# Kernel tuning notes

Measured on AMD Instinct MI355X. Metric: run time of the kernel, lower is better.

Reference implementation:

```python
import jax, jax.numpy as jnp
import numpy as np

D_MODEL = 1024
NUM_HEADS = 16
D_K = D_MODEL // NUM_HEADS


def setup_inputs() -> dict:
    key = jax.random.key(0)
    ks = jax.random.split(key, 7)
    B, S = 2, 2048
    scale = 1.0 / np.sqrt(D_MODEL)
    return {
        "Q": jax.random.normal(ks[0], (B, S, D_MODEL), dtype=jnp.float32),
        "K": jax.random.normal(ks[1], (B, S, D_MODEL), dtype=jnp.float32),
        "V": jax.random.normal(ks[2], (B, S, D_MODEL), dtype=jnp.float32),
        "W_q": jax.random.normal(ks[3], (D_MODEL, D_MODEL), dtype=jnp.float32) * scale,
        "W_k": jax.random.normal(ks[4], (D_MODEL, D_MODEL), dtype=jnp.float32) * scale,
        "W_v": jax.random.normal(ks[5], (D_MODEL, D_MODEL), dtype=jnp.float32) * scale,
        "W_o": jax.random.normal(ks[6], (D_MODEL, D_MODEL), dtype=jnp.float32) * scale,
    }


def _split_heads(x):
    B, S, _ = x.shape
    return x.reshape(B, S, NUM_HEADS, D_K).transpose(0, 2, 1, 3)  # [B,H,S,Dk]


def reference(Q, K, V, W_q, W_k, W_v, W_o):
    # nn.Linear(bias=False): x @ W.T
    q = _split_heads(Q @ W_q.T)
    k = _split_heads(K @ W_k.T)
    v = _split_heads(V @ W_v.T)
    scores = jnp.einsum("bhqd,bhkd->bhqk", q, k) / jnp.sqrt(jnp.float32(D_K))
    probs = jax.nn.softmax(scores, axis=-1)
    out = jnp.einsum("bhqk,bhkd->bhqd", probs, v)  # [B,H,S,Dk]
    B, H, S, Dk = out.shape
    out = out.transpose(0, 2, 1, 3).reshape(B, S, H * Dk)
    return out @ W_o.T
```

## Files before the change

kernel.cpp:

```cpp
#include <hip/hip_runtime.h>
#include <cstdint>

#define D_MODEL 1024
#define NH 16
#define DK 64
#define SEQ 2048
#define BATCH 2
#define M_TOT (BATCH * SEQ)

typedef __bf16 bf16x8          __attribute__((ext_vector_type(8)));
typedef unsigned short u16x8   __attribute__((ext_vector_type(8)));
typedef float  f32x4           __attribute__((ext_vector_type(4)));

union pun8 { u16x8 u; bf16x8 b; };

__device__ __forceinline__ f32x4 mfma16(bf16x8 a, bf16x8 b, f32x4 c) {
    return __builtin_amdgcn_mfma_f32_16x16x32_bf16(a, b, c, 0, 0, 0);
}

__device__ __forceinline__ unsigned short f2bf(float f) {
    union { float f; uint32_t u; } v; v.f = f;
    uint32_t u = v.u;
    return (unsigned short)((u + 0x7FFFu + ((u >> 16) & 1u)) >> 16);
}

__device__ __forceinline__ unsigned short f2bf_trunc(float f) {
    union { float f; uint32_t u; } v; v.f = f;
    return (unsigned short)(v.u >> 16);
}

__device__ __forceinline__ void gl_lds16(const unsigned short* g, unsigned short* l) {
    __builtin_amdgcn_global_load_lds(
        (const __attribute__((address_space(1))) void*)g,
        (__attribute__((address_space(3))) void*)l, 16, 0, 0);
}

#define C_EXP2 0.1803368801111204f

__global__ __launch_bounds__(256) void convert_all_kernel(
    const float* __restrict__ Q,  const float* __restrict__ K,
    const float* __restrict__ V,  const float* __restrict__ Wq,
    const float* __restrict__ Wk, const float* __restrict__ Wv,
    const float* __restrict__ Wo,
    unsigned short* __restrict__ Qb,  unsigned short* __restrict__ Kb,
    unsigned short* __restrict__ Vb,  unsigned short* __restrict__ Wqb,
    unsigned short* __restrict__ Wkb, unsigned short* __restrict__ Wvb,
    unsigned short* __restrict__ Wob)
{
    int bid = blockIdx.x;
    const float* src; unsigned short* dst; int base;
    if (bid < 3 * 2048) {
        int r = bid >> 11;
        src  = (r == 0) ? Q  : (r == 1) ? K  : V;
        dst  = (r == 0) ? Qb : (r == 1) ? Kb : Vb;
        base = (bid & 2047) * 2048;
    } else {
        int u = bid - 3 * 2048;
        int r = u >> 9;
        src  = (r == 0) ? Wq  : (r == 1) ? Wk  : (r == 2) ? Wv  : Wo;
        dst  = (r == 0) ? Wqb : (r == 1) ? Wkb : (r == 2) ? Wvb : Wob;
        base = (u & 511) * 2048;
    }
    int i = base + threadIdx.x * 8;
    float4 a = *(const float4*)(src + i);
    float4 b = *(const float4*)(src + i + 4);
    u16x8 o;
    o[0] = f2bf(a.x); o[1] = f2bf(a.y); o[2] = f2bf(a.z); o[3] = f2bf(a.w);
    o[4] = f2bf(b.x); o[5] = f2bf(b.y); o[6] = f2bf(b.z); o[7] = f2bf(b.w);
    *(u16x8*)(dst + i) = o;
}

__global__ __launch_bounds__(256) void qkv_proj_kernel(
    const unsigned short* __restrict__ Q,
    const unsigned short* __restrict__ K,
    const unsigned short* __restrict__ V,
    const unsigned short* __restrict__ Wq,
    const unsigned short* __restrict__ Wk,
    const unsigned short* __restrict__ Wv,
    unsigned short* __restrict__ qb,
    unsigned short* __restrict__ kb,
    unsigned short* __restrict__ vtb)
{
    const int z = blockIdx.z;
    const unsigned short* A  = (z == 0) ? Q  : (z == 1) ? K  : V;
    const unsigned short* Bt = (z == 0) ? Wq : (z == 1) ? Wk : Wv;

    const int m0 = blockIdx.y * 128;
    const int n0 = blockIdx.x * 128;

    __shared__ __align__(16) unsigned short smem[128 * 136];
    unsigned short* As = smem;
    unsigned short* Bs = smem + 128 * 64;
    unsigned short* Cs = smem;

    const int t    = threadIdx.x;
    const int lane = t & 63;
    const int w    = t >> 6;
    const int l15  = lane & 15;
    const int quad = lane >> 4;
    const int wm   = (w >> 1) * 64;
    const int wn   = (w & 1) * 64;

    f32x4 acc[4][4] = {};

    for (int k0 = 0; k0 < D_MODEL; k0 += 64) {
        __syncthreads();
        #pragma unroll
        for (int i = 0; i < 4; i++) {
            int u   = t + i * 256;
            int row = u >> 3;
            int kc  = (u & 7) * 8;
            gl_lds16(&A [(m0 + row) * D_MODEL + k0 + kc], &As[(i * 256 + w * 64) * 8]);
            gl_lds16(&Bt[(n0 + row) * D_MODEL + k0 + kc], &Bs[(i * 256 + w * 64) * 8]);
        }
        __syncthreads();

        #pragma unroll
        for (int kk = 0; kk < 2; kk++) {
            bf16x8 a[4], b[4];
            #pragma unroll
            for (int mi = 0; mi < 4; mi++)
                a[mi] = *(const bf16x8*)(&As[(wm + mi * 16 + l15) * 64 + kk * 32 + quad * 8]);
            #pragma unroll
            for (int ni = 0; ni < 4; ni++)
                b[ni] = *(const bf16x8*)(&Bs[(wn + ni * 16 + l15) * 64 + kk * 32 + quad * 8]);

            #pragma unroll
            for (int mi = 0; mi < 4; mi++)
                #pragma unroll
                for (int ni = 0; ni < 4; ni++)
                    acc[mi][ni] = mfma16(a[mi], b[ni], acc[mi][ni]);
        }
    }

    const float oscale = (z == 0) ? C_EXP2 : 1.0f;
    __syncthreads();
    #pragma unroll
    for (int mi = 0; mi < 4; mi++) {
        #pragma unroll
        for (int ni = 0; ni < 4; ni++) {
            #pragma unroll
            for (int r = 0; r < 4; r++) {
                int rloc = wm + mi * 16 + quad * 4 + r;
                int cloc = wn + ni * 16 + l15;
                int rr = (z == 2) ? cloc : rloc;
                int cc = (z == 2) ? rloc : cloc;
                Cs[rr * 136 + cc] = f2bf(acc[mi][ni][r] * oscale);
            }
        }
    }
    __syncthreads();
    #pragma unroll
    for (int i = 0; i < 8; i++) {
        int u    = t + i * 256;
        int rrow = u >> 4;
        int cc8  = (u & 15) * 8;
        u16x8 val = *(const u16x8*)(&Cs[rrow * 136 + cc8]);
        unsigned short* dst;
        if (z < 2) {
            int m = m0 + rrow, n = n0 + cc8;
            int bi = m >> 11, s = m & (SEQ - 1);
            int hh = n >> 6,  d = n & (DK - 1);
            dst = ((z == 0) ? qb : kb) + (((size_t)(bi * NH + hh) * SEQ + s) * DK + d);
        } else {
            int dglob = n0 + rrow;
            int bi = m0 >> 11, s = (m0 & (SEQ - 1)) + cc8;
            int hh = dglob >> 6, d = dglob & (DK - 1);
            dst = vtb + (((size_t)(bi * NH + hh) * DK + d) * SEQ + s);
        }
        *(u16x8*)dst = val;
    }
}

__global__ __launch_bounds__(256, 2) void attn_kernel(
    const unsigned short* __restrict__ qb,
    const unsigned short* __restrict__ kb,
    const unsigned short* __restrict__ vtb,
    unsigned short* __restrict__ ctx)
{
    const int h  = blockIdx.x;
    const int qt = blockIdx.y;
    const int b  = blockIdx.z;

    const int t    = threadIdx.x;
    const int lane = t & 63;
    const int w    = t >> 6;
    const int l15  = lane & 15;
    const int quad = lane >> 4;

    const unsigned short* qh = qb  + ((b * NH + h) * SEQ) * DK;
    const unsigned short* kh = kb  + ((b * NH + h) * SEQ) * DK;
    const unsigned short* vh = vtb + ((b * NH + h) * DK) * SEQ;

    __shared__ __align__(16) unsigned short p_lds[4][32][72];
    __shared__ __align__(16) unsigned short Ks[128 * 72];
    __shared__ __align__(16) unsigned short Vs[64 * 136];

    const int qrow0 = qt * 128 + w * 32;
    bf16x8 qa[2][2];
    #pragma unroll
    for (int m = 0; m < 2; m++)
        #pragma unroll
        for (int kk = 0; kk < 2; kk++)
            qa[m][kk] = *(const bf16x8*)(&qh[(qrow0 + m * 16 + l15) * DK + kk * 32 + quad * 8]);

    pun8 ones_p;
    #pragma unroll
    for (int i = 0; i < 8; i++) ones_p.u[i] = 0x3F80;
    const bf16x8 ones = ones_p.b;

    f32x4 o[2][4] = {};
    f32x4 lacc[2] = {};

    bf16x8 pa_p[2][2] = {};
    bf16x8 vf_p[4][2] = {};

    for (int kt = 0; kt < SEQ / 128; kt++) {
        __syncthreads();
        #pragma unroll
        for (int i = 0; i < 4; i++) {
            int u   = t + i * 256;
            int row = u >> 3;
            int c8  = (u & 7) * 8;
            *(u16x8*)(&Ks[row * 72 + c8]) =
                *(const u16x8*)(&kh[(kt * 128 + row) * DK + c8]);
        }
        #pragma unroll
        for (int i = 0; i < 4; i++) {
            int u   = t + i * 256;
            int row = u >> 4;
            int c8  = (u & 15) * 8;
            *(u16x8*)(&Vs[row * 136 + c8]) =
                *(const u16x8*)(&vh[row * SEQ + kt * 128 + c8]);
        }
        __syncthreads();

        #pragma unroll
        for (int hh = 0; hh < 2; hh++) {
            bf16x8 kf[4][2];
            #pragma unroll
            for (int nb = 0; nb < 4; nb++) {
                const int krow = hh * 64 + nb * 16 + l15;
                kf[nb][0] = *(const bf16x8*)(&Ks[krow * 72 + quad * 8]);
                kf[nb][1] = *(const bf16x8*)(&Ks[krow * 72 + 32 + quad * 8]);
            }

            f32x4 sacc[2][4] = {};
            __builtin_amdgcn_s_setprio(1);
            #pragma unroll
            for (int m = 0; m < 2; m++)
                #pragma unroll
                for (int nb = 0; nb < 4; nb++) {
                    sacc[m][nb] = mfma16(qa[m][0], kf[nb][0], sacc[m][nb]);
                    sacc[m][nb] = mfma16(qa[m][1], kf[nb][1], sacc[m][nb]);
                }
            __builtin_amdgcn_s_setprio(0);

            bf16x8 vf_c[4][2];
            #pragma unroll
            for (int db = 0; db < 4; db++) {
                vf_c[db][0] = *(const bf16x8*)(&Vs[(db * 16 + l15) * 136 + hh * 64 + quad * 8]);
                vf_c[db][1] = *(const bf16x8*)(&Vs[(db * 16 + l15) * 136 + hh * 64 + 32 + quad * 8]);
            }

            __builtin_amdgcn_s_setprio(1);
            #pragma unroll
            for (int db = 0; db < 4; db++)
                #pragma unroll
                for (int m = 0; m < 2; m++) {
                    o[m][db] = mfma16(pa_p[m][0], vf_p[db][0], o[m][db]);
                    o[m][db] = mfma16(pa_p[m][1], vf_p[db][1], o[m][db]);
                }
            #pragma unroll
            for (int m = 0; m < 2; m++) {
                lacc[m] = mfma16(pa_p[m][0], ones, lacc[m]);
                lacc[m] = mfma16(pa_p[m][1], ones, lacc[m]);
            }
            __builtin_amdgcn_s_setprio(0);

            #pragma unroll
            for (int m = 0; m < 2; m++)
                #pragma unroll
                for (int nb = 0; nb < 4; nb++)
                    #pragma unroll
                    for (int r = 0; r < 4; r++) {
                        float p = exp2f(sacc[m][nb][r]);
                        p_lds[w][m * 16 + quad * 4 + r][nb * 16 + l15] = f2bf_trunc(p);
                    }

            asm volatile("" ::: "memory");

            #pragma unroll
            for (int m = 0; m < 2; m++)
                #pragma unroll
                for (int kk = 0; kk < 2; kk++)
                    pa_p[m][kk] = *(const bf16x8*)(&p_lds[w][m * 16 + l15][kk * 32 + quad * 8]);

            asm volatile("" ::: "memory");

            #pragma unroll
            for (int db = 0; db < 4; db++) {
                vf_p[db][0] = vf_c[db][0];
                vf_p[db][1] = vf_c[db][1];
            }
        }
    }

    __builtin_amdgcn_s_setprio(1);
    #pragma unroll
    for (int db = 0; db < 4; db++)
        #pragma unroll
        for (int m = 0; m < 2; m++) {
            o[m][db] = mfma16(pa_p[m][0], vf_p[db][0], o[m][db]);
            o[m][db] = mfma16(pa_p[m][1], vf_p[db][1], o[m][db]);
        }
    #pragma unroll
    for (int m = 0; m < 2; m++) {
        lacc[m] = mfma16(pa_p[m][0], ones, lacc[m]);
        lacc[m] = mfma16(pa_p[m][1], ones, lacc[m]);
    }
    __builtin_amdgcn_s_setprio(0);

    #pragma unroll
    for (int m = 0; m < 2; m++) {
        const int srow_base = b * SEQ + qt * 128 + w * 32 + m * 16 + quad * 4;
        #pragma unroll
        for (int db = 0; db < 4; db++)
            #pragma unroll
            for (int r = 0; r < 4; r++) {
                float val = o[m][db][r] / lacc[m][r];
                ctx[(srow_base + r) * D_MODEL + h * DK + db * 16 + l15] = f2bf(val);
            }
    }
}

__global__ __launch_bounds__(256) void out_proj_kernel(
    const unsigned short* __restrict__ A,
    const unsigned short* __restrict__ Bt,
    float* __restrict__ out)
{
    const int m0 = blockIdx.y * 64;
    const int n0 = blockIdx.x * 128;

    __shared__ __align__(16) unsigned short As[64 * 64];
    __shared__ __align__(16) unsigned short Bs[128 * 64];

    const int t    = threadIdx.x;
    const int lane = t & 63;
    const int w    = t >> 6;
    const int l15  = lane & 15;
    const int quad = lane >> 4;
    const int wn   = w * 32;

    f32x4 acc[4][2] = {};

    for (int k0 = 0; k0 < D_MODEL; k0 += 64) {
        __syncthreads();
        #pragma unroll
        for (int i = 0; i < 2; i++) {
            int u   = t + i * 256;
            int row = u >> 3;
            int kc  = (u & 7) * 8;
            gl_lds16(&A[(m0 + row) * D_MODEL + k0 + kc], &As[(i * 256 + w * 64) * 8]);
        }
        #pragma unroll
        for (int i = 0; i < 4; i++) {
            int u   = t + i * 256;
            int row = u >> 3;
            int kc  = (u & 7) * 8;
            gl_lds16(&Bt[(n0 + row) * D_MODEL + k0 + kc], &Bs[(i * 256 + w * 64) * 8]);
        }
        __syncthreads();

        #pragma unroll
        for (int kk = 0; kk < 2; kk++) {
            bf16x8 a[4], bfr[2];
            #pragma unroll
            for (int mi = 0; mi < 4; mi++)
                a[mi] = *(const bf16x8*)(&As[(mi * 16 + l15) * 64 + kk * 32 + quad * 8]);
            #pragma unroll
            for (int ni = 0; ni < 2; ni++)
                bfr[ni] = *(const bf16x8*)(&Bs[(wn + ni * 16 + l15) * 64 + kk * 32 + quad * 8]);

            #pragma unroll
            for (int mi = 0; mi < 4; mi++)
                #pragma unroll
                for (int ni = 0; ni < 2; ni++)
                    acc[mi][ni] = mfma16(a[mi], bfr[ni], acc[mi][ni]);
        }
    }

    #pragma unroll
    for (int mi = 0; mi < 4; mi++) {
        #pragma unroll
        for (int ni = 0; ni < 2; ni++) {
            #pragma unroll
            for (int r = 0; r < 4; r++) {
                int m = m0 + mi * 16 + quad * 4 + r;
                int n = n0 + wn + ni * 16 + l15;
                out[m * D_MODEL + n] = acc[mi][ni][r];
            }
        }
    }
}

extern "C" void kernel_launch(void* const* d_in, const int* in_sizes, int n_in,
                              void* d_out, int out_size, void* d_ws, size_t ws_size,
                              hipStream_t stream) {
    const float* Q  = (const float*)d_in[0];
    const float* K  = (const float*)d_in[1];
    const float* V  = (const float*)d_in[2];
    const float* Wq = (const float*)d_in[3];
    const float* Wk = (const float*)d_in[4];
    const float* Wv = (const float*)d_in[5];
    const float* Wo = (const float*)d_in[6];

    const size_t NQ = (size_t)M_TOT * D_MODEL;
    const size_t NW = (size_t)D_MODEL * D_MODEL;

    unsigned short* Qb  = (unsigned short*)d_ws;
    unsigned short* Kb  = Qb  + NQ;
    unsigned short* Vb  = Kb  + NQ;
    unsigned short* Wqb = Vb  + NQ;
    unsigned short* Wkb = Wqb + NW;
    unsigned short* Wvb = Wkb + NW;
    unsigned short* Wob = Wvb + NW;
    unsigned short* qb  = Wob + NW;
    unsigned short* kbf = qb  + NQ;
    unsigned short* vtb = kbf + NQ;
    unsigned short* ctx = vtb + NQ;
    float* out = (float*)d_out;

    convert_all_kernel<<<3 * 2048 + 4 * 512, 256, 0, stream>>>(
        Q, K, V, Wq, Wk, Wv, Wo, Qb, Kb, Vb, Wqb, Wkb, Wvb, Wob);

    dim3 g1(D_MODEL / 128, M_TOT / 128, 3);
    qkv_proj_kernel<<<g1, 256, 0, stream>>>(Qb, Kb, Vb, Wqb, Wkb, Wvb, qb, kbf, vtb);

    dim3 g2(NH, SEQ / 128, BATCH);
    attn_kernel<<<g2, 256, 0, stream>>>(qb, kbf, vtb, ctx);

    dim3 g3(D_MODEL / 128, M_TOT / 64, 1);
    out_proj_kernel<<<g3, 256, 0, stream>>>(ctx, Wob, out);
}
```

Before: 230.8 us.

## Split attention KV range in two and merge partials in output projection

```diff
diff --git a/kernel.cpp b/kernel.cpp
--- a/kernel.cpp
+++ b/kernel.cpp
@@ -27,6 +27,11 @@
 __device__ __forceinline__ unsigned short f2bf_trunc(float f) {
     union { float f; uint32_t u; } v; v.f = f;
     return (unsigned short)(v.u >> 16);
+}
+
+__device__ __forceinline__ float bf2f(unsigned short s) {
+    union { uint32_t u; float f; } v; v.u = ((uint32_t)s) << 16;
+    return v.f;
 }
 
 __device__ __forceinline__ void gl_lds16(const unsigned short* g, unsigned short* l) {
@@ -176,11 +181,16 @@
     const unsigned short* __restrict__ qb,
     const unsigned short* __restrict__ kb,
     const unsigned short* __restrict__ vtb,
-    unsigned short* __restrict__ ctx)
+    unsigned short* __restrict__ u0,
+    unsigned short* __restrict__ u1,
+    float* __restrict__ l0,
+    float* __restrict__ l1)
 {
     const int h  = blockIdx.x;
     const int qt = blockIdx.y;
-    const int b  = blockIdx.z;
+    const int zb = blockIdx.z;
+    const int b  = zb >> 1;
+    const int g  = zb & 1;
 
     const int t    = threadIdx.x;
     const int lane = t & 63;
@@ -188,13 +198,13 @@
     const int l15  = lane & 15;
     const int quad = lane >> 4;
 
-    const unsigned short* qh = qb  + ((b * NH + h) * SEQ) * DK;
-    const unsigned short* kh = kb  + ((b * NH + h) * SEQ) * DK;
-    const unsigned short* vh = vtb + ((b * NH + h) * DK) * SEQ;
+    const unsigned short* qh = qb  + ((size_t)(b * NH + h) * SEQ) * DK;
+    const unsigned short* kh = kb  + ((size_t)(b * NH + h) * SEQ + g * (SEQ / 2)) * DK;
+    const unsigned short* vh = vtb + ((size_t)(b * NH + h) * DK) * SEQ + g * (SEQ / 2);
 
     __shared__ __align__(16) unsigned short p_lds[4][32][72];
-    __shared__ __align__(16) unsigned short Ks[128 * 72];
-    __shared__ __align__(16) unsigned short Vs[64 * 136];
+    __shared__ __align__(16) unsigned short Ks[64 * 72];
+    __shared__ __align__(16) unsigned short Vs[64 * 72];
 
     const int qrow0 = qt * 128 + w * 32;
     bf16x8 qa[2][2];
@@ -215,94 +225,91 @@
     bf16x8 pa_p[2][2] = {};
     bf16x8 vf_p[4][2] = {};
 
-    for (int kt = 0; kt < SEQ / 128; kt++) {
-        __syncthreads();
-        #pragma unroll
-        for (int i = 0; i < 4; i++) {
+    for (int kt = 0; kt < 16; kt++) {
+        __syncthreads();
+        #pragma unroll
+        for (int i = 0; i < 2; i++) {
             int u   = t + i * 256;
             int row = u >> 3;
             int c8  = (u & 7) * 8;
             *(u16x8*)(&Ks[row * 72 + c8]) =
-                *(const u16x8*)(&kh[(kt * 128 + row) * DK + c8]);
-        }
-        #pragma unroll
-        for (int i = 0; i < 4; i++) {
+                *(const u16x8*)(&kh[(kt * 64 + row) * DK + c8]);
+        }
+        #pragma unroll
+        for (int i = 0; i < 2; i++) {
             int u   = t + i * 256;
-            int row = u >> 4;
-            int c8  = (u & 15) * 8;
-            *(u16x8*)(&Vs[row * 136 + c8]) =
-                *(const u16x8*)(&vh[row * SEQ + kt * 128 + c8]);
-        }
-        __syncthreads();
-
-        #pragma unroll
-        for (int hh = 0; hh < 2; hh++) {
-            bf16x8 kf[4][2];
+            int row = u >> 3;
+            int c8  = (u & 7) * 8;
+            *(u16x8*)(&Vs[row * 72 + c8]) =
+                *(const u16x8*)(&vh[row * SEQ + kt * 64 + c8]);
+        }
+        __syncthreads();
+
+        bf16x8 kf[4][2];
+        #pragma unroll
+        for (int nb = 0; nb < 4; nb++) {
+            const int krow = nb * 16 + l15;
+            kf[nb][0] = *(const bf16x8*)(&Ks[krow * 72 + quad * 8]);
+            kf[nb][1] = *(const bf16x8*)(&Ks[krow * 72 + 32 + quad * 8]);
+        }
+
+        f32x4 sacc[2][4] = {};
+        __builtin_amdgcn_s_setprio(1);
+        #pragma unroll
+        for (int m = 0; m < 2; m++)
             #pragma unroll
             for (int nb = 0; nb < 4; nb++) {
-                const int krow = hh * 64 + nb * 16 + l15;
-                kf[nb][0] = *(const bf16x8*)(&Ks[krow * 72 + quad * 8]);
-                kf[nb][1] = *(const bf16x8*)(&Ks[krow * 72 + 32 + quad * 8]);
+                sacc[m][nb] = mfma16(qa[m][0], kf[nb][0], sacc[m][nb]);
+                sacc[m][nb] = mfma16(qa[m][1], kf[nb][1], sacc[m][nb]);
             }
-
-            f32x4 sacc[2][4] = {};
-            __builtin_amdgcn_s_setprio(1);
-            #pragma unroll
-            for (int m = 0; m < 2; m++)
+        __builtin_amdgcn_s_setprio(0);
+
+        bf16x8 vf_c[4][2];
+        #pragma unroll
+        for (int db = 0; db < 4; db++) {
+            vf_c[db][0] = *(const bf16x8*)(&Vs[(db * 16 + l15) * 72 + quad * 8]);
+            vf_c[db][1] = *(const bf16x8*)(&Vs[(db * 16 + l15) * 72 + 32 + quad * 8]);
+        }
+
+        __builtin_amdgcn_s_setprio(1);
+        #pragma unroll
+        for (int db = 0; db < 4; db++)
+            #pragma unroll
+            for (int m = 0; m < 2; m++) {
+                o[m][db] = mfma16(pa_p[m][0], vf_p[db][0], o[m][db]);
+                o[m][db] = mfma16(pa_p[m][1], vf_p[db][1], o[m][db]);
+            }
+        #pragma unroll
+        for (int m = 0; m < 2; m++) {
+            lacc[m] = mfma16(pa_p[m][0], ones, lacc[m]);
+            lacc[m] = mfma16(pa_p[m][1], ones, lacc[m]);
+        }
+        __builtin_amdgcn_s_setprio(0);
+
+        #pragma unroll
+        for (int m = 0; m < 2; m++)
+            #pragma unroll
+            for (int nb = 0; nb < 4; nb++)
                 #pragma unroll
-                for (int nb = 0; nb < 4; nb++) {
-                    sacc[m][nb] = mfma16(qa[m][0], kf[nb][0], sacc[m][nb]);
-                    sacc[m][nb] = mfma16(qa[m][1], kf[nb][1], sacc[m][nb]);
+                for (int r = 0; r < 4; r++) {
+                    float p = exp2f(sacc[m][nb][r]);
+                    p_lds[w][m * 16 + quad * 4 + r][nb * 16 + l15] = f2bf_trunc(p);
                 }
-            __builtin_amdgcn_s_setprio(0);
-
-            bf16x8 vf_c[4][2];
-            #pragma unroll
-            for (int db = 0; db < 4; db++) {
-                vf_c[db][0] = *(const bf16x8*)(&Vs[(db * 16 + l15) * 136 + hh * 64 + quad * 8]);
-                vf_c[db][1] = *(const bf16x8*)(&Vs[(db * 16 + l15) * 136 + hh * 64 + 32 + quad * 8]);
-            }
-
-            __builtin_amdgcn_s_setprio(1);
-            #pragma unroll
-            for (int db = 0; db < 4; db++)
-                #pragma unroll
-                for (int m = 0; m < 2; m++) {
-                    o[m][db] = mfma16(pa_p[m][0], vf_p[db][0], o[m][db]);
-                    o[m][db] = mfma16(pa_p[m][1], vf_p[db][1], o[m][db]);
-                }
-            #pragma unroll
-            for (int m = 0; m < 2; m++) {
-                lacc[m] = mfma16(pa_p[m][0], ones, lacc[m]);
-                lacc[m] = mfma16(pa_p[m][1], ones, lacc[m]);
-            }
-            __builtin_amdgcn_s_setprio(0);
-
-            #pragma unroll
-            for (int m = 0; m < 2; m++)
-                #pragma unroll
-                for (int nb = 0; nb < 4; nb++)
-                    #pragma unroll
-                    for (int r = 0; r < 4; r++) {
-                        float p = exp2f(sacc[m][nb][r]);
-                        p_lds[w][m * 16 + quad * 4 + r][nb * 16 + l15] = f2bf_trunc(p);
-                    }
-
-            asm volatile("" ::: "memory");
-
-            #pragma unroll
-            for (int m = 0; m < 2; m++)
-                #pragma unroll
-                for (int kk = 0; kk < 2; kk++)
-                    pa_p[m][kk] = *(const bf16x8*)(&p_lds[w][m * 16 + l15][kk * 32 + quad * 8]);
-
-            asm volatile("" ::: "memory");
-
-            #pragma unroll
-            for (int db = 0; db < 4; db++) {
-                vf_p[db][0] = vf_c[db][0];
-                vf_p[db][1] = vf_c[db][1];
-            }
+
+        asm volatile("" ::: "memory");
+
+        #pragma unroll
+        for (int m = 0; m < 2; m++)
+            #pragma unroll
+            for (int kk = 0; kk < 2; kk++)
+                pa_p[m][kk] = *(const bf16x8*)(&p_lds[w][m * 16 + l15][kk * 32 + quad * 8]);
+
+        asm volatile("" ::: "memory");
+
+        #pragma unroll
+        for (int db = 0; db < 4; db++) {
+            vf_p[db][0] = vf_c[db][0];
+            vf_p[db][1] = vf_c[db][1];
         }
     }
 
@@ -321,21 +328,32 @@
     }
     __builtin_amdgcn_s_setprio(0);
 
+    unsigned short* ug = g ? u1 : u0;
+    float*          lg = g ? l1 : l0;
     #pragma unroll
     for (int m = 0; m < 2; m++) {
-        const int srow_base = b * SEQ + qt * 128 + w * 32 + m * 16 + quad * 4;
+        const int srow = qt * 128 + w * 32 + m * 16 + quad * 4;
         #pragma unroll
         for (int db = 0; db < 4; db++)
             #pragma unroll
             for (int r = 0; r < 4; r++) {
                 float val = o[m][db][r] / lacc[m][r];
-                ctx[(srow_base + r) * D_MODEL + h * DK + db * 16 + l15] = f2bf(val);
+                ug[(size_t)(b * SEQ + srow + r) * D_MODEL + h * DK + db * 16 + l15] =
+                    f2bf(val);
             }
+        if (l15 == 0) {
+            #pragma unroll
+            for (int r = 0; r < 4; r++)
+                lg[(size_t)(b * NH + h) * SEQ + srow + r] = lacc[m][r];
+        }
     }
 }
 
 __global__ __launch_bounds__(256) void out_proj_kernel(
-    const unsigned short* __restrict__ A,
+    const unsigned short* __restrict__ u0,
+    const unsigned short* __restrict__ u1,
+    const float* __restrict__ l0,
+    const float* __restrict__ l1,
     const unsigned short* __restrict__ Bt,
     float* __restrict__ out)
 {
@@ -360,8 +378,21 @@
         for (int i = 0; i < 2; i++) {
             int u   = t + i * 256;
             int row = u >> 3;
-            int kc  = (u & 7) * 8;
-            gl_lds16(&A[(m0 + row) * D_MODEL + k0 + kc], &As[(i * 256 + w * 64) * 8]);
+            int c8  = (u & 7) * 8;
+            int mg  = m0 + row;
+            int bb  = mg >> 11, ss = mg & (SEQ - 1);
+            int hh  = (k0 + c8) >> 6;
+            float la = l0[(size_t)(bb * NH + hh) * SEQ + ss];
+            float lb = l1[(size_t)(bb * NH + hh) * SEQ + ss];
+            float inv = 1.0f / (la + lb);
+            float wa = la * inv, wb = lb * inv;
+            u16x8 a0 = *(const u16x8*)(&u0[(size_t)mg * D_MODEL + k0 + c8]);
+            u16x8 a1 = *(const u16x8*)(&u1[(size_t)mg * D_MODEL + k0 + c8]);
+            u16x8 o8;
+            #pragma unroll
+            for (int j = 0; j < 8; j++)
+                o8[j] = f2bf(wa * bf2f(a0[j]) + wb * bf2f(a1[j]));
+            *(u16x8*)(&As[row * 64 + c8]) = o8;
         }
         #pragma unroll
         for (int i = 0; i < 4; i++) {
@@ -428,8 +459,12 @@
     unsigned short* qb  = Wob + NW;
     unsigned short* kbf = qb  + NQ;
     unsigned short* vtb = kbf + NQ;
-    unsigned short* ctx = vtb + NQ;
     float* out = (float*)d_out;
+
+    unsigned short* u0p = Qb;
+    unsigned short* u1p = Kb;
+    float* l0p = (float*)Vb;
+    float* l1p = (float*)(Vb + 1024 * 1024);
 
     convert_all_kernel<<<3 * 2048 + 4 * 512, 256, 0, stream>>>(
         Q, K, V, Wq, Wk, Wv, Wo, Qb, Kb, Vb, Wqb, Wkb, Wvb, Wob);
@@ -437,9 +472,9 @@
     dim3 g1(D_MODEL / 128, M_TOT / 128, 3);
     qkv_proj_kernel<<<g1, 256, 0, stream>>>(Qb, Kb, Vb, Wqb, Wkb, Wvb, qb, kbf, vtb);
 
-    dim3 g2(NH, SEQ / 128, BATCH);
-    attn_kernel<<<g2, 256, 0, stream>>>(qb, kbf, vtb, ctx);
+    dim3 g2(NH, SEQ / 128, 2 * BATCH);
+    attn_kernel<<<g2, 256, 0, stream>>>(qb, kbf, vtb, u0p, u1p, l0p, l1p);
 
     dim3 g3(D_MODEL / 128, M_TOT / 64, 1);
-    out_proj_kernel<<<g3, 256, 0, stream>>>(ctx, Wob, out);
-}
+    out_proj_kernel<<<g3, 256, 0, stream>>>(u0p, u1p, l0p, l1p, Wob, out);
+}
```

Measured after the change: 260.1 us. 12.7% more time.
